# Performance work log

Hardware: AMD Instinct MI355X
Metric: run time of the kernel (lower is better)

The kernel has to match this reference:

```python
import jax, jax.numpy as jnp
import numpy as np

N_SRC, N_DST, E, R = 50000, 10000, 250000, 4
IN, OUT, H, DH = 256, 256, 4, 64  # DH = OUT // H
NEG_SLOPE = 0.2  # DGL GATConv default LeakyReLU slope


def setup_inputs() -> dict:
    key = jax.random.key(0)
    ks = jax.random.split(key, 8)
    x = jax.random.normal(ks[0], (N_SRC, IN), jnp.float32)
    W = jax.random.normal(ks[1], (R, IN, OUT), jnp.float32) / np.sqrt(IN).astype(np.float32)
    attn_l = jax.random.normal(ks[2], (R, H, DH), jnp.float32) * 0.1
    attn_r = jax.random.normal(ks[3], (R, H, DH), jnp.float32) * 0.1
    loop_w = jax.random.normal(ks[4], (IN, OUT), jnp.float32) / np.sqrt(IN).astype(np.float32)
    loop_b = jnp.zeros((OUT,), jnp.float32)
    edge_src = jax.random.randint(ks[5], (R, E), 0, N_SRC, dtype=jnp.int32)
    edge_dst = jax.random.randint(ks[6], (R, E), 0, N_DST, dtype=jnp.int32)
    return dict(x=x, W=W, attn_l=attn_l, attn_r=attn_r, loop_w=loop_w,
                loop_b=loop_b, edge_src=edge_src, edge_dst=edge_dst, n_dst=N_DST)


def _gat_rel(x, Wr, al, ar, src, dst, n_dst):
    """One DGL-style GATConv (shared fc for src/dst, no bias, zero-in-degree ok)."""
    n_heads, dh = al.shape
    h = (x @ Wr).reshape(-1, n_heads, dh)            # [N_src, H, DH]
    el = jnp.sum(h * al, axis=-1)                    # [N_src, H]
    er = jnp.sum(h[:n_dst] * ar, axis=-1)            # [N_dst, H]
    e = jax.nn.leaky_relu(el[src] + er[dst], negative_slope=NEG_SLOPE)  # [E, H]
    # segment softmax over incoming edges of each dst node (numerically stable)
    emax = jax.ops.segment_max(e, dst, num_segments=n_dst)
    emax = jnp.where(jnp.isfinite(emax), emax, jnp.float32(0))  # empty segments
    ex = jnp.exp(e - emax[dst])                      # [E, H]
    denom = jax.ops.segment_sum(ex, dst, num_segments=n_dst)
    alpha = ex / jnp.maximum(denom[dst], jnp.float32(1e-9))     # [E, H]
    msg = h[src] * alpha[:, :, None]                 # [E, H, DH]
    out = jax.ops.segment_sum(msg, dst, num_segments=n_dst)     # [N_dst, H, DH]
    return out.reshape(n_dst, n_heads * dh)


def reference(x, W, attn_l, attn_r, loop_w, loop_b, edge_src, edge_dst, n_dst):
    n_rel = W.shape[0]
    agg = jnp.zeros((n_dst, OUT), jnp.float32)
    for r in range(n_rel):  # fixed small set of relation-specific convs
        agg = agg + _gat_rel(x, W[r], attn_l[r], attn_r[r],
                             edge_src[r], edge_dst[r], n_dst)
    agg = agg / jnp.float32(n_rel)                   # stack(...).mean(0)
    h = x[:n_dst] @ loop_w + loop_b + agg            # residual loop_weights
    return jax.nn.relu(h)                            # activation; dropout=0
```

## Files before the change

### kernel.cpp

```cpp
#include <hip/hip_runtime.h>

#define NSRC 50000
#define NDST 10000
#define NEDGE 250000
#define NREL 4
#define NEG_SLOPE 0.2f
#define EMAXC 128
#define NSEG (NREL * NDST)
#define NBLK 32
#define CHUNK 7813

typedef unsigned short u16;
typedef __attribute__((ext_vector_type(8))) short bf16x8;
typedef __attribute__((ext_vector_type(4))) float f32x4;
typedef __attribute__((ext_vector_type(2))) float f32x2;

#define GLD16(g, l) __builtin_amdgcn_global_load_lds( \
    (__attribute__((address_space(1))) void*)(void*)(g), \
    (__attribute__((address_space(3))) void*)(l), 16, 0, 0)

static __device__ __forceinline__ u16 f2b(float f) {
  unsigned u = __float_as_uint(f);
  unsigned r = (u + 0x7FFFu + ((u >> 16) & 1u)) >> 16;
  return (u16)r;
}
static __device__ __forceinline__ float b2f(u16 b) {
  return __uint_as_float((unsigned)b << 16);
}
static __device__ __forceinline__ float leaky(float x) {
  return x > 0.f ? x : NEG_SLOPE * x;
}

static __device__ __forceinline__ unsigned enc8_sw(float f) {
  unsigned s = (__float_as_uint(f) >> 24) & 0x80u;
  float a = fminf(fabsf(f), 448.f);
  unsigned em;
  if (a < 0x1p-6f) {
    em = (unsigned)rintf(a * 512.f);
  } else {
    unsigned ab = __float_as_uint(a);
    unsigned lsb = (ab >> 20) & 1u;
    ab += 0x7FFFFu + lsb;
    int e = (int)(ab >> 23) - 127;
    unsigned m = (ab >> 20) & 7u;
    em = (unsigned)((e + 7) << 3) | m;
    if (em > 0x7Eu) em = 0x7Eu;
  }
  return s | em;
}
static __device__ __forceinline__ float dec8_sw(unsigned b) {
  unsigned s = b & 0x80u;
  unsigned em = b & 0x7Fu;
  float n = __uint_as_float((s << 24) | ((em << 20) + 0x3C000000u));
  float sub = (s ? -1.f : 1.f) * (float)em * 0x1p-9f;
  return em >= 8 ? n : sub;
}
static __device__ __forceinline__ unsigned enc4(float a, float b, float c, float d) {
#if __has_builtin(__builtin_amdgcn_cvt_pk_fp8_f32)
  int q = __builtin_amdgcn_cvt_pk_fp8_f32(a, b, 0, 0);
  q = __builtin_amdgcn_cvt_pk_fp8_f32(c, d, q, 1);
  return (unsigned)q;
#else
  return enc8_sw(a) | (enc8_sw(b) << 8) | (enc8_sw(c) << 16) | (enc8_sw(d) << 24);
#endif
}
static __device__ __forceinline__ void dec4(unsigned q, float f[4]) {
#if __has_builtin(__builtin_amdgcn_cvt_pk_f32_fp8)
  f32x2 lo = __builtin_amdgcn_cvt_pk_f32_fp8((int)q, 0);
  f32x2 hi = __builtin_amdgcn_cvt_pk_f32_fp8((int)q, 1);
  f[0] = lo.x; f[1] = lo.y; f[2] = hi.x; f[3] = hi.y;
#else
  f[0] = dec8_sw(q & 0xff); f[1] = dec8_sw((q >> 8) & 0xff);
  f[2] = dec8_sw((q >> 16) & 0xff); f[3] = dec8_sw(q >> 24);
#endif
}
static __device__ __forceinline__ unsigned pk_bf16(float a, float b) {
  unsigned r;
  asm("v_cvt_pk_bf16_f32 %0, %1, %2" : "=v"(r) : "v"(a), "v"(b));
  return r;
}
static __device__ __forceinline__ uint4 dec8_bf16(unsigned q0, unsigned q1) {
  float f[8];
  dec4(q0, f);
  dec4(q1, f + 4);
  uint4 o;
  o.x = pk_bf16(f[0], f[1]);
  o.y = pk_bf16(f[2], f[3]);
  o.z = pk_bf16(f[4], f[5]);
  o.w = pk_bf16(f[6], f[7]);
  return o;
}

#define CB_CVTX 1563
#define CB_WBL  160
#define CB_WA   16
#define NGRP 3200000

__global__ __launch_bounds__(256) void prep_k(const float* __restrict__ x,
                                              const float* __restrict__ W,
                                              const float* __restrict__ loop_w,
                                              const float* __restrict__ al,
                                              const float* __restrict__ ar,
                                              u16* __restrict__ xb,
                                              unsigned* __restrict__ xq,
                                              u16* __restrict__ WBL,
                                              u16* __restrict__ WAt) {
  const int bi = blockIdx.x;
  const int tid = threadIdx.x;
  if (bi < CB_CVTX) {
    const int base = bi * 2048 + tid;
    float4 v[8];
    #pragma unroll
    for (int it = 0; it < 8; ++it) {
      int i = base + it * 256;
      if (i < NGRP) v[it] = ((const float4*)x)[i];
    }
    #pragma unroll
    for (int it = 0; it < 8; ++it) {
      int i = base + it * 256;
      if (i < NGRP) {
        uint2 o;
        o.x = (unsigned)f2b(v[it].x) | ((unsigned)f2b(v[it].y) << 16);
        o.y = (unsigned)f2b(v[it].z) | ((unsigned)f2b(v[it].w) << 16);
        ((uint2*)xb)[i] = o;
        xq[i] = enc4(v[it].x, v[it].y, v[it].z, v[it].w);
      }
    }
  } else if (bi < CB_CVTX + CB_WBL) {
    const int g0 = (bi - CB_CVTX) * 2048 + tid;
    float v[8];
    #pragma unroll
    for (int it = 0; it < 8; ++it) {
      int g = g0 + it * 256;
      int h = g / 81920, rem = g - h * 81920;
      int np = rem / 1280, kp = rem - np * 1280;
      if (kp < 1024)
        v[it] = 0.25f * W[(size_t)(kp >> 8) * 65536 + (size_t)(kp & 255) * 256 + h * 64 + np];
      else
        v[it] = loop_w[(size_t)(kp - 1024) * 256 + h * 64 + np];
    }
    #pragma unroll
    for (int it = 0; it < 8; ++it) WBL[g0 + it * 256] = f2b(v[it]);
  } else {
    const int g0 = (bi - CB_CVTX - CB_WBL) * 2048 + tid;
    #pragma unroll
    for (int it = 0; it < 8; ++it) {
      int g = g0 + it * 256;
      int c = g >> 8, k = g & 255;
      float acc = 0.f;
      if (c < 32) {
        int cc = c & 15;
        int r = cc >> 2, h = cc & 3;
        const float* vec = ((c < 16) ? al : ar) + r * 256 + h * 64;
        const float* wrow = W + (size_t)r * 65536 + (size_t)k * 256 + h * 64;
        #pragma unroll 8
        for (int j = 0; j < 64; ++j) acc += wrow[j] * vec[j];
      }
      WAt[(size_t)c * 256 + k] = f2b(acc);
    }
  }
}

__global__ __launch_bounds__(256) void histrank_k(const int* __restrict__ edst,
                                                  u16* __restrict__ ranks,
                                                  unsigned* __restrict__ bhist) {
  __shared__ unsigned lh[NDST];
  const int bi = blockIdx.x, r = blockIdx.y;
  for (int i = threadIdx.x; i < NDST; i += 256) lh[i] = 0;
  __syncthreads();
  const int base = bi * CHUNK;
  const int lim = (NEDGE - base < CHUNK) ? (NEDGE - base) : CHUNK;
  const int* ed = edst + (size_t)r * NEDGE + base;
  u16* rk = ranks + (size_t)r * NEDGE + base;
  for (int i = threadIdx.x; i < lim; i += 256) {
    int d = ed[i];
    rk[i] = (u16)atomicAdd(&lh[d], 1u);
  }
  __syncthreads();
  unsigned* bh = bhist + ((size_t)r * NBLK + bi) * NDST;
  for (int i = threadIdx.x; i < NDST; i += 256) bh[i] = lh[i];
}

__global__ __launch_bounds__(256) void scanbb_k(unsigned* __restrict__ bhist,
                                                int* __restrict__ counts) {
  int gid = blockIdx.x * 256 + threadIdx.x;
  if (gid >= NSEG) return;
  int r = gid / NDST, bin = gid - r * NDST;
  unsigned run = 0;
  unsigned* base = bhist + (size_t)r * NBLK * NDST + bin;
  #pragma unroll
  for (int b = 0; b < NBLK; ++b) {
    unsigned v = base[(size_t)b * NDST];
    base[(size_t)b * NDST] = run;
    run += v;
  }
  counts[gid] = (int)run;
}

__global__ void place_k(const int* __restrict__ esrc, const int* __restrict__ edst,
                        const u16* __restrict__ ranks,
                        const unsigned* __restrict__ bhist,
                        const int* __restrict__ offs, int* __restrict__ perm) {
  int g = blockIdx.x * 256 + threadIdx.x;
  if (g >= NREL * NEDGE) return;
  int r = g / NEDGE, e = g - r * NEDGE;
  int bi = e / CHUNK;
  int d = edst[g];
  int pos = offs[r * NDST + d] +
            (int)bhist[((size_t)r * NBLK + bi) * NDST + d] + (int)ranks[g];
  perm[pos] = esrc[g];
}

__global__ __launch_bounds__(1024) void scanA_k(const int* __restrict__ counts,
                                                int* __restrict__ offsets,
                                                int* __restrict__ btot) {
  __shared__ int wsum[16];
  int tid = threadIdx.x, lane = tid & 63, wid = tid >> 6;
  int i = blockIdx.x * 1024 + tid;
  int v = (i < NSEG) ? counts[i] : 0;
  int x = v;
  #pragma unroll
  for (int off = 1; off < 64; off <<= 1) {
    int t = __shfl_up(x, off);
    if (lane >= off) x += t;
  }
  if (lane == 63) wsum[wid] = x;
  __syncthreads();
  if (wid == 0) {
    int t = (lane < 16) ? wsum[lane] : 0;
    #pragma unroll
    for (int off = 1; off < 16; off <<= 1) {
      int u = __shfl_up(t, off);
      if (lane >= off) t += u;
    }
    if (lane < 16) wsum[lane] = t;
  }
  __syncthreads();
  int wpre = (wid > 0) ? wsum[wid - 1] : 0;
  int incl = x + wpre;
  if (i < NSEG) offsets[i] = incl - v;
  if (tid == 1023) btot[blockIdx.x] = incl;
}

__global__ void scanB_k(const int* __restrict__ btot, int* __restrict__ carry) {
  int lane = threadIdx.x;
  int v = (lane < 40) ? btot[lane] : 0;
  int x = v;
  #pragma unroll
  for (int off = 1; off < 64; off <<= 1) {
    int t = __shfl_up(x, off);
    if (lane >= off) x += t;
  }
  if (lane < 40) carry[lane] = x - v;
}

__global__ __launch_bounds__(1024) void scanC_k(int* __restrict__ offsets,
                                                const int* __restrict__ carry) {
  int i = blockIdx.x * 1024 + threadIdx.x;
  if (i < NSEG) offsets[i] += carry[blockIdx.x];
  if (i == 0) offsets[NSEG] = NREL * NEDGE;
}

__global__ __launch_bounds__(256) void gemmE_k(const u16* __restrict__ A,
                                               const u16* __restrict__ B,
                                               float* __restrict__ outF) {
  __shared__ u16 As[128 * 64];
  __shared__ u16 Bs[32 * 64];
  const int tid = threadIdx.x;
  const int w = tid >> 6, l = tid & 63;
  const int bm = blockIdx.y * 128;
  const int wm = w * 32;
  f32x4 acc[2][2] = {};
  const int lrow = l >> 3, lchunk = l & 7;

  for (int t = 0; t < 4; ++t) {
    const int k0 = t * 64;
    #pragma unroll
    for (int c = 0; c < 4; ++c) {
      int rb = (w * 4 + c) * 8;
      int row_in = rb + lrow;
      int colb = (lchunk * 16) ^ ((row_in & 7) << 4);
      long arow = bm + row_in;
      if (arow >= NSRC) arow = NSRC - 1;
      const char* ga = (const char*)A + ((size_t)arow * 256 + k0) * 2 + colb;
      GLD16(ga, (char*)As + rb * 128);
    }
    {
      int rb = w * 8;
      int row_in = rb + lrow;
      int colb = (lchunk * 16) ^ ((row_in & 7) << 4);
      const char* gb = (const char*)B + ((size_t)row_in * 256 + k0) * 2 + colb;
      GLD16(gb, (char*)Bs + rb * 128);
    }
    __syncthreads();
    #pragma unroll
    for (int kk = 0; kk < 2; ++kk) {
      bf16x8 af[2], bg[2];
      #pragma unroll
      for (int m = 0; m < 2; ++m) {
        int row = wm + m * 16 + (l & 15);
        int colb = (kk * 64 + ((l >> 4) * 16)) ^ ((row & 7) << 4);
        af[m] = *(const bf16x8*)((const char*)As + row * 128 + colb);
      }
      #pragma unroll
      for (int n = 0; n < 2; ++n) {
        int row = n * 16 + (l & 15);
        int colb = (kk * 64 + ((l >> 4) * 16)) ^ ((row & 7) << 4);
        bg[n] = *(const bf16x8*)((const char*)Bs + row * 128 + colb);
      }
      #pragma unroll
      for (int m = 0; m < 2; ++m)
        #pragma unroll
        for (int n = 0; n < 2; ++n)
          acc[m][n] = __builtin_amdgcn_mfma_f32_16x16x32_bf16(af[m], bg[n], acc[m][n], 0, 0, 0);
    }
    __syncthreads();
  }
  #pragma unroll
  for (int m = 0; m < 2; ++m) {
    #pragma unroll
    for (int j = 0; j < 4; ++j) {
      int row = bm + wm + m * 16 + (l >> 4) * 4 + j;
      if (row < NSRC) {
        #pragma unroll
        for (int n = 0; n < 2; ++n) {
          int col = n * 16 + (l & 15);
          outF[(size_t)row * 32 + col] = acc[m][n][j];
        }
      }
    }
  }
}

__global__ __launch_bounds__(256) void gemmF_k(const unsigned* __restrict__ xaggQ,
                                               const u16* __restrict__ xb,
                                               const u16* __restrict__ WBL,
                                               const float* __restrict__ loop_b,
                                               float* __restrict__ out) {
  __shared__ u16 As[128 * 64];
  __shared__ u16 Bs[64 * 64];
  const int tid = threadIdx.x;
  const int w = tid >> 6, l = tid & 63;
  const int h = blockIdx.z;
  const int bm = blockIdx.y * 128;
  const int wm = w * 32;
  const char* A1 = (const char*)xaggQ + (size_t)h * NDST * 1024;
  const u16* Bh = WBL + (size_t)h * 64 * 1280;
  f32x4 acc[2][4] = {};
  const int lrow = l >> 3, lchunk = l & 7;

  for (int t = 0; t < 20; ++t) {
    const int k0 = t * 64;
    if (t < 16) {
      int row_in = tid >> 1, half = tid & 1;
      long arow = bm + row_in;
      if (arow >= NDST) arow = NDST - 1;
      const uint4* gsrc = (const uint4*)(A1 + (size_t)arow * 1024 + k0 + half * 32);
      uint4 qa = gsrc[0];
      uint4 qb = gsrc[1];
      uint4 c0 = dec8_bf16(qa.x, qa.y);
      uint4 c1 = dec8_bf16(qa.z, qa.w);
      uint4 c2 = dec8_bf16(qb.x, qb.y);
      uint4 c3 = dec8_bf16(qb.z, qb.w);
      char* rowp = (char*)As + row_in * 128;
      const int sw = (row_in & 7) << 4;
      *(uint4*)(rowp + ((half * 64 + 0) ^ sw))  = c0;
      *(uint4*)(rowp + ((half * 64 + 16) ^ sw)) = c1;
      *(uint4*)(rowp + ((half * 64 + 32) ^ sw)) = c2;
      *(uint4*)(rowp + ((half * 64 + 48) ^ sw)) = c3;
    } else {
      #pragma unroll
      for (int c = 0; c < 4; ++c) {
        int rb = (w * 4 + c) * 8;
        int row_in = rb + lrow;
        int colb = (lchunk * 16) ^ ((row_in & 7) << 4);
        long arow = bm + row_in;
        if (arow >= NDST) arow = NDST - 1;
        const char* ga = (const char*)xb + ((size_t)arow * 256 + (k0 - 1024)) * 2 + colb;
        GLD16(ga, (char*)As + rb * 128);
      }
    }
    #pragma unroll
    for (int c = 0; c < 2; ++c) {
      int rb = (w * 2 + c) * 8;
      int row_in = rb + lrow;
      int colb = (lchunk * 16) ^ ((row_in & 7) << 4);
      const char* gb = (const char*)Bh + ((size_t)row_in * 1280 + k0) * 2 + colb;
      GLD16(gb, (char*)Bs + rb * 128);
    }
    __syncthreads();
    #pragma unroll
    for (int kk = 0; kk < 2; ++kk) {
      bf16x8 af[2], bg[4];
      #pragma unroll
      for (int m = 0; m < 2; ++m) {
        int row = wm + m * 16 + (l & 15);
        int colb = (kk * 64 + ((l >> 4) * 16)) ^ ((row & 7) << 4);
        af[m] = *(const bf16x8*)((const char*)As + row * 128 + colb);
      }
      #pragma unroll
      for (int n = 0; n < 4; ++n) {
        int row = n * 16 + (l & 15);
        int colb = (kk * 64 + ((l >> 4) * 16)) ^ ((row & 7) << 4);
        bg[n] = *(const bf16x8*)((const char*)Bs + row * 128 + colb);
      }
      #pragma unroll
      for (int m = 0; m < 2; ++m)
        #pragma unroll
        for (int n = 0; n < 4; ++n)
          acc[m][n] = __builtin_amdgcn_mfma_f32_16x16x32_bf16(af[m], bg[n], acc[m][n], 0, 0, 0);
    }
    __syncthreads();
  }
  #pragma unroll
  for (int m = 0; m < 2; ++m) {
    #pragma unroll
    for (int j = 0; j < 4; ++j) {
      int row = bm + wm + m * 16 + (l >> 4) * 4 + j;
      if (row < NDST) {
        #pragma unroll
        for (int n = 0; n < 4; ++n) {
          int col = n * 16 + (l & 15);
          out[(size_t)row * 256 + h * 64 + col] =
              fmaxf(acc[m][n][j] + loop_b[h * 64 + col], 0.f);
        }
      }
    }
  }
}

static __device__ __forceinline__ void edge_fma(float (&ac)[4][4], float4 a4, unsigned q) {
  float f[4];
  dec4(q, f);
  const float ah[4] = {a4.x, a4.y, a4.z, a4.w};
  #pragma unroll
  for (int h = 0; h < 4; ++h)
    #pragma unroll
    for (int c = 0; c < 4; ++c)
      ac[h][c] = fmaf(ah[h], f[c], ac[h][c]);
}

__global__ __launch_bounds__(64) void agg_k(const unsigned* __restrict__ xq,
                                            const int* __restrict__ offs,
                                            const int* __restrict__ perm,
                                            const float* __restrict__ elr,
                                            unsigned* __restrict__ xaggQ) {
  __shared__ float sex[EMAXC][4];
  const int d = blockIdx.x;
  const int r = blockIdx.y;
  const int lane = threadIdx.x;
  const int seg = r * NDST + d;
  const int beg = offs[seg], end = offs[seg + 1];
  const int n = end - beg;
  const float4 r4 = *(const float4*)(elr + (size_t)d * 32 + 16 + r * 4);

  float s0 = 0.f, s1 = 0.f, s2 = 0.f, s3 = 0.f;
  for (int e = lane; e < n; e += 64) {
    int s = perm[beg + e];
    float4 l4 = *(const float4*)(elr + (size_t)s * 32 + r * 4);
    float e0 = __expf(leaky(l4.x + r4.x));
    float e1 = __expf(leaky(l4.y + r4.y));
    float e2 = __expf(leaky(l4.z + r4.z));
    float e3 = __expf(leaky(l4.w + r4.w));
    if (e < EMAXC) *(float4*)&sex[e][0] = make_float4(e0, e1, e2, e3);
    s0 += e0; s1 += e1; s2 += e2; s3 += e3;
  }
  #pragma unroll
  for (int off = 1; off < 64; off <<= 1) {
    s0 += __shfl_xor(s0, off);
    s1 += __shfl_xor(s1, off);
    s2 += __shfl_xor(s2, off);
    s3 += __shfl_xor(s3, off);
  }
  const float rd0 = 1.f / fmaxf(s0, 1e-9f);
  const float rd1 = 1.f / fmaxf(s1, 1e-9f);
  const float rd2 = 1.f / fmaxf(s2, 1e-9f);
  const float rd3 = 1.f / fmaxf(s3, 1e-9f);
  for (int e = lane; e < n && e < EMAXC; e += 64) {
    float4 v = *(const float4*)&sex[e][0];
    *(float4*)&sex[e][0] = make_float4(v.x * rd0, v.y * rd1, v.z * rd2, v.w * rd3);
  }
  __syncthreads();

  float ac[4][4] = {};
  const int nc = (n < EMAXC) ? n : EMAXC;
  int e = 0;
  for (; e + 3 < nc; e += 4) {
    int sA = perm[beg + e], sB = perm[beg + e + 1];
    int sC = perm[beg + e + 2], sD = perm[beg + e + 3];
    float4 aA = *(const float4*)&sex[e][0];
    float4 aB = *(const float4*)&sex[e + 1][0];
    float4 aC = *(const float4*)&sex[e + 2][0];
    float4 aD = *(const float4*)&sex[e + 3][0];
    unsigned qA = xq[(size_t)sA * 64 + lane];
    unsigned qB = xq[(size_t)sB * 64 + lane];
    unsigned qC = xq[(size_t)sC * 64 + lane];
    unsigned qD = xq[(size_t)sD * 64 + lane];
    edge_fma(ac, aA, qA);
    edge_fma(ac, aB, qB);
    edge_fma(ac, aC, qC);
    edge_fma(ac, aD, qD);
  }
  for (; e < nc; ++e) {
    int s = perm[beg + e];
    float4 aa = *(const float4*)&sex[e][0];
    unsigned q = xq[(size_t)s * 64 + lane];
    edge_fma(ac, aa, q);
  }
  for (int i = EMAXC; i < n; ++i) {
    int s = perm[beg + i];
    float4 l4 = *(const float4*)(elr + (size_t)s * 32 + r * 4);
    float4 aa;
    aa.x = __expf(leaky(l4.x + r4.x)) * rd0;
    aa.y = __expf(leaky(l4.y + r4.y)) * rd1;
    aa.z = __expf(leaky(l4.z + r4.z)) * rd2;
    aa.w = __expf(leaky(l4.w + r4.w)) * rd3;
    unsigned q = xq[(size_t)s * 64 + lane];
    edge_fma(ac, aa, q);
  }

  #pragma unroll
  for (int h = 0; h < 4; ++h) {
    xaggQ[((size_t)h * NDST + d) * 256 + (size_t)r * 64 + lane] =
        enc4(ac[h][0], ac[h][1], ac[h][2], ac[h][3]);
  }
}

extern "C" void kernel_launch(void* const* d_in, const int* in_sizes, int n_in,
                              void* d_out, int out_size, void* d_ws, size_t ws_size,
                              hipStream_t stream) {
  const float* x      = (const float*)d_in[0];
  const float* W      = (const float*)d_in[1];
  const float* attn_l = (const float*)d_in[2];
  const float* attn_r = (const float*)d_in[3];
  const float* loop_w = (const float*)d_in[4];
  const float* loop_b = (const float*)d_in[5];
  const int* edge_src = (const int*)d_in[6];
  const int* edge_dst = (const int*)d_in[7];
  float* out = (float*)d_out;

  char* wsp = (char*)d_ws;
  size_t off = 0;
  auto alloc = [&](size_t bytes) -> char* {
    char* p = wsp + off;
    off = (off + bytes + 255) & ~(size_t)255;
    return p;
  };
  u16* xb        = (u16*)alloc((size_t)NSRC * 256 * 2);
  unsigned* xq   = (unsigned*)alloc((size_t)NSRC * 64 * 4);
  u16* WBL       = (u16*)alloc((size_t)4 * 64 * 1280 * 2);
  u16* WAt       = (u16*)alloc((size_t)128 * 256 * 2);
  float* elr     = (float*)alloc((size_t)NSRC * 32 * 4);
  unsigned* xaggQ= (unsigned*)alloc((size_t)4 * NDST * 256 * 4);
  u16* ranks     = (u16*)alloc((size_t)NREL * NEDGE * 2);
  unsigned* bh   = (unsigned*)alloc((size_t)NREL * NBLK * NDST * 4);
  int* counts    = (int*)alloc((size_t)NSEG * 4);
  int* offs      = (int*)alloc((size_t)(NSEG + 1) * 4);
  int* btot      = (int*)alloc(64 * 4);
  int* carry     = (int*)alloc(64 * 4);
  int* perm      = (int*)alloc((size_t)NREL * NEDGE * 4);

  prep_k<<<CB_CVTX + CB_WBL + CB_WA, 256, 0, stream>>>(
      x, W, loop_w, attn_l, attn_r, xb, xq, WBL, WAt);

  histrank_k<<<dim3(NBLK, NREL), 256, 0, stream>>>(edge_dst, ranks, bh);
  scanbb_k<<<(NSEG + 255) / 256, 256, 0, stream>>>(bh, counts);
  scanA_k<<<40, 1024, 0, stream>>>(counts, offs, btot);
  scanB_k<<<1, 64, 0, stream>>>(btot, carry);
  scanC_k<<<40, 1024, 0, stream>>>(offs, carry);
  place_k<<<(NREL * NEDGE + 255) / 256, 256, 0, stream>>>(
      edge_src, edge_dst, ranks, bh, offs, perm);

  gemmE_k<<<dim3(1, (NSRC + 127) / 128), 256, 0, stream>>>(xb, WAt, elr);

  agg_k<<<dim3(NDST, NREL), 64, 0, stream>>>(xq, offs, perm, elr, xaggQ);

  gemmF_k<<<dim3(1, (NDST + 127) / 128, 4), 256, 0, stream>>>(
      xaggQ, xb, WBL, loop_b, out);
}
```

Measured before the change: 160.2 us.

## Replace three-kernel scan with per-relation single-block scan; pack agg FMAs

```diff
diff --git a/kernel.cpp b/kernel.cpp
--- a/kernel.cpp
+++ b/kernel.cpp
@@ -64,15 +64,19 @@
   return enc8_sw(a) | (enc8_sw(b) << 8) | (enc8_sw(c) << 16) | (enc8_sw(d) << 24);
 #endif
 }
+static __device__ __forceinline__ void dec4v(unsigned q, f32x2& lo, f32x2& hi) {
+#if __has_builtin(__builtin_amdgcn_cvt_pk_f32_fp8)
+  lo = __builtin_amdgcn_cvt_pk_f32_fp8((int)q, 0);
+  hi = __builtin_amdgcn_cvt_pk_f32_fp8((int)q, 1);
+#else
+  lo = (f32x2){dec8_sw(q & 0xff), dec8_sw((q >> 8) & 0xff)};
+  hi = (f32x2){dec8_sw((q >> 16) & 0xff), dec8_sw(q >> 24)};
+#endif
+}
 static __device__ __forceinline__ void dec4(unsigned q, float f[4]) {
-#if __has_builtin(__builtin_amdgcn_cvt_pk_f32_fp8)
-  f32x2 lo = __builtin_amdgcn_cvt_pk_f32_fp8((int)q, 0);
-  f32x2 hi = __builtin_amdgcn_cvt_pk_f32_fp8((int)q, 1);
+  f32x2 lo, hi;
+  dec4v(q, lo, hi);
   f[0] = lo.x; f[1] = lo.y; f[2] = hi.x; f[3] = hi.y;
-#else
-  f[0] = dec8_sw(q & 0xff); f[1] = dec8_sw((q >> 8) & 0xff);
-  f[2] = dec8_sw((q >> 16) & 0xff); f[3] = dec8_sw(q >> 24);
-#endif
 }
 static __device__ __forceinline__ unsigned pk_bf16(float a, float b) {
   unsigned r;
@@ -197,6 +201,49 @@
   counts[gid] = (int)run;
 }
 
+__global__ __launch_bounds__(1024) void scan4_k(const int* __restrict__ counts,
+                                                int* __restrict__ offsets) {
+  __shared__ int wsum[16];
+  const int r = blockIdx.x;
+  const int tid = threadIdx.x, lane = tid & 63, wid = tid >> 6;
+  const int base = tid * 10;
+  int loc[10];
+  int s = 0;
+  #pragma unroll
+  for (int i = 0; i < 10; ++i) {
+    int idx = base + i;
+    int v = (idx < NDST) ? counts[r * NDST + idx] : 0;
+    s += v;
+    loc[i] = s;
+  }
+  int x = s;
+  #pragma unroll
+  for (int off = 1; off < 64; off <<= 1) {
+    int t = __shfl_up(x, off);
+    if (lane >= off) x += t;
+  }
+  if (lane == 63) wsum[wid] = x;
+  __syncthreads();
+  if (wid == 0) {
+    int t = (lane < 16) ? wsum[lane] : 0;
+    #pragma unroll
+    for (int off = 1; off < 16; off <<= 1) {
+      int u = __shfl_up(t, off);
+      if (lane >= off) t += u;
+    }
+    if (lane < 16) wsum[lane] = t;
+  }
+  __syncthreads();
+  int wpre = (wid > 0) ? wsum[wid - 1] : 0;
+  int gbase = r * NEDGE + wpre + x - s;
+  #pragma unroll
+  for (int i = 0; i < 10; ++i) {
+    int idx = base + i;
+    if (idx < NDST) offsets[r * NDST + idx] = gbase + (i ? loc[i - 1] : 0);
+  }
+  if (tid == 1023 && r == NREL - 1) offsets[NSEG] = NREL * NEDGE;
+}
+
 __global__ void place_k(const int* __restrict__ esrc, const int* __restrict__ edst,
                         const u16* __restrict__ ranks,
                         const unsigned* __restrict__ bhist,
@@ -209,56 +256,6 @@
   int pos = offs[r * NDST + d] +
             (int)bhist[((size_t)r * NBLK + bi) * NDST + d] + (int)ranks[g];
   perm[pos] = esrc[g];
-}
-
-__global__ __launch_bounds__(1024) void scanA_k(const int* __restrict__ counts,
-                                                int* __restrict__ offsets,
-                                                int* __restrict__ btot) {
-  __shared__ int wsum[16];
-  int tid = threadIdx.x, lane = tid & 63, wid = tid >> 6;
-  int i = blockIdx.x * 1024 + tid;
-  int v = (i < NSEG) ? counts[i] : 0;
-  int x = v;
-  #pragma unroll
-  for (int off = 1; off < 64; off <<= 1) {
-    int t = __shfl_up(x, off);
-    if (lane >= off) x += t;
-  }
-  if (lane == 63) wsum[wid] = x;
-  __syncthreads();
-  if (wid == 0) {
-    int t = (lane < 16) ? wsum[lane] : 0;
-    #pragma unroll
-    for (int off = 1; off < 16; off <<= 1) {
-      int u = __shfl_up(t, off);
-      if (lane >= off) t += u;
-    }
-    if (lane < 16) wsum[lane] = t;
-  }
-  __syncthreads();
-  int wpre = (wid > 0) ? wsum[wid - 1] : 0;
-  int incl = x + wpre;
-  if (i < NSEG) offsets[i] = incl - v;
-  if (tid == 1023) btot[blockIdx.x] = incl;
-}
-
-__global__ void scanB_k(const int* __restrict__ btot, int* __restrict__ carry) {
-  int lane = threadIdx.x;
-  int v = (lane < 40) ? btot[lane] : 0;
-  int x = v;
-  #pragma unroll
-  for (int off = 1; off < 64; off <<= 1) {
-    int t = __shfl_up(x, off);
-    if (lane >= off) x += t;
-  }
-  if (lane < 40) carry[lane] = x - v;
-}
-
-__global__ __launch_bounds__(1024) void scanC_k(int* __restrict__ offsets,
-                                                const int* __restrict__ carry) {
-  int i = blockIdx.x * 1024 + threadIdx.x;
-  if (i < NSEG) offsets[i] += carry[blockIdx.x];
-  if (i == 0) offsets[NSEG] = NREL * NEDGE;
 }
 
 __global__ __launch_bounds__(256) void gemmE_k(const u16* __restrict__ A,
@@ -429,15 +426,16 @@
   }
 }
 
-static __device__ __forceinline__ void edge_fma(float (&ac)[4][4], float4 a4, unsigned q) {
-  float f[4];
-  dec4(q, f);
+static __device__ __forceinline__ void edge_fma(f32x2 (&ac)[4][2], float4 a4, unsigned q) {
+  f32x2 lo, hi;
+  dec4v(q, lo, hi);
   const float ah[4] = {a4.x, a4.y, a4.z, a4.w};
   #pragma unroll
-  for (int h = 0; h < 4; ++h)
-    #pragma unroll
-    for (int c = 0; c < 4; ++c)
-      ac[h][c] = fmaf(ah[h], f[c], ac[h][c]);
+  for (int h = 0; h < 4; ++h) {
+    f32x2 av = {ah[h], ah[h]};
+    ac[h][0] += av * lo;
+    ac[h][1] += av * hi;
+  }
 }
 
 __global__ __launch_bounds__(64) void agg_k(const unsigned* __restrict__ xq,
@@ -482,7 +480,7 @@
   }
   __syncthreads();
 
-  float ac[4][4] = {};
+  f32x2 ac[4][2] = {};
   const int nc = (n < EMAXC) ? n : EMAXC;
   int e = 0;
   for (; e + 3 < nc; e += 4) {
@@ -522,7 +520,7 @@
   #pragma unroll
   for (int h = 0; h < 4; ++h) {
     xaggQ[((size_t)h * NDST + d) * 256 + (size_t)r * 64 + lane] =
-        enc4(ac[h][0], ac[h][1], ac[h][2], ac[h][3]);
+        enc4(ac[h][0].x, ac[h][0].y, ac[h][1].x, ac[h][1].y);
   }
 }
 
@@ -556,8 +554,6 @@
   unsigned* bh   = (unsigned*)alloc((size_t)NREL * NBLK * NDST * 4);
   int* counts    = (int*)alloc((size_t)NSEG * 4);
   int* offs      = (int*)alloc((size_t)(NSEG + 1) * 4);
-  int* btot      = (int*)alloc(64 * 4);
-  int* carry     = (int*)alloc(64 * 4);
   int* perm      = (int*)alloc((size_t)NREL * NEDGE * 4);
 
   prep_k<<<CB_CVTX + CB_WBL + CB_WA, 256, 0, stream>>>(
@@ -565,9 +561,7 @@
 
   histrank_k<<<dim3(NBLK, NREL), 256, 0, stream>>>(edge_dst, ranks, bh);
   scanbb_k<<<(NSEG + 255) / 256, 256, 0, stream>>>(bh, counts);
-  scanA_k<<<40, 1024, 0, stream>>>(counts, offs, btot);
-  scanB_k<<<1, 64, 0, stream>>>(btot, carry);
-  scanC_k<<<40, 1024, 0, stream>>>(offs, carry);
+  scan4_k<<<NREL, 1024, 0, stream>>>(counts, offs);
   place_k<<<(NREL * NEDGE + 255) / 256, 256, 0, stream>>>(
       edge_src, edge_dst, ranks, bh, offs, perm);
 
```

New measurement: 161.0 us. Within noise of the previous version (+0.5%).
